# Optimization experiments

Measured on AMD Instinct MI355X. Metric: run time of the kernel, lower is better.

Reference implementation:

```python
import jax, jax.numpy as jnp
import numpy as np

B, T, D_IN, D_OUT = 2, 2048, 2048, 2048
H, KV = 32, 8
HD = D_OUT // H          # 64
G = H // KV              # group_size = 4
ROPE_BASE = 10000.0


def setup_inputs() -> dict:
    key = jax.random.key(0)
    ks = jax.random.split(key, 5)
    s = 0.02  # weight init scale
    return {
        "x":  jax.random.normal(ks[0], (B, T, D_IN), jnp.float32),
        "Wq": jax.random.normal(ks[1], (D_IN, D_OUT), jnp.float32) * s,
        "Wk": jax.random.normal(ks[2], (D_IN, KV * HD), jnp.float32) * s,
        "Wv": jax.random.normal(ks[3], (D_IN, KV * HD), jnp.float32) * s,
        "Wo": jax.random.normal(ks[4], (D_OUT, D_OUT), jnp.float32) * s,
    }


def _rope_cos_sin(t, hd):
    inv = 1.0 / (ROPE_BASE ** (jnp.arange(0, hd, 2, dtype=jnp.float32) / hd))
    ang = jnp.arange(t, dtype=jnp.float32)[:, None] * inv[None, :]  # (T, hd/2)
    return jnp.cos(ang), jnp.sin(ang)


def _apply_rope(x, cos, sin):
    # x: (b, h, T, hd); rotate adjacent pairs (complex multiply, Llama-style)
    xr = x.reshape(x.shape[:-1] + (HD // 2, 2))
    x0, x1 = xr[..., 0], xr[..., 1]
    c = cos[None, None]  # (1,1,T,hd/2)
    s = sin[None, None]
    o0 = x0 * c - x1 * s
    o1 = x0 * s + x1 * c
    return jnp.stack([o0, o1], axis=-1).reshape(x.shape)


def reference(x, Wq, Wk, Wv, Wo):
    b, t, _ = x.shape
    q = (x @ Wq).reshape(b, t, H, HD).transpose(0, 2, 1, 3)    # (b,H,T,hd)
    k = (x @ Wk).reshape(b, t, KV, HD).transpose(0, 2, 1, 3)   # (b,KV,T,hd)
    v = (x @ Wv).reshape(b, t, KV, HD).transpose(0, 2, 1, 3)
    cos, sin = _rope_cos_sin(t, HD)
    q = _apply_rope(q, cos, sin)
    k = _apply_rope(k, cos, sin)
    # GQA: expand KV groups to all heads (repeat_interleave on head dim)
    k = jnp.repeat(k, G, axis=1)  # (b,H,T,hd)
    v = jnp.repeat(v, G, axis=1)
    scores = jnp.einsum('bhqd,bhkd->bhqk', q, k) / jnp.sqrt(jnp.float32(HD))
    causal = jnp.triu(jnp.ones((t, t), dtype=bool), 1)
    scores = jnp.where(causal[None, None], -jnp.inf, scores)
    w = jax.nn.softmax(scores, axis=-1)
    ctx = jnp.einsum('bhqk,bhkd->bqhd', w, v).reshape(b, t, D_OUT)
    return ctx @ Wo
```

## Files before the change

kernel.cpp:

```cpp
#include <hip/hip_runtime.h>

#define TQ 2048
#define NB 2
#define NH 32
#define NKV 8
#define HD 64
#define DIN 2048
#define DOUT 2048
#define NQKV 3072
#define QK_W 2560
#define GK 2048

typedef unsigned short u16;
typedef unsigned int u32;
typedef __attribute__((ext_vector_type(8))) short bf16x8;
typedef __attribute__((ext_vector_type(4))) float f32x4;
typedef __attribute__((ext_vector_type(4))) u16 u16x4;

typedef __attribute__((address_space(1))) const u32 gas_u32;
typedef __attribute__((address_space(3))) u32 las_u32;

#define NEG (-1.0e30f)

__device__ __forceinline__ u16 f2bf(float f) {
  u32 u = __float_as_uint(f);
  u += 0x7fffu + ((u >> 16) & 1u);
  return (u16)(u >> 16);
}
__device__ __forceinline__ float bf2f(u16 h) { return __uint_as_float(((u32)h) << 16); }
__device__ __forceinline__ u32 pack2(float lo, float hi) {
  return (u32)f2bf(lo) | ((u32)f2bf(hi) << 16);
}

__global__ __launch_bounds__(256)
void k_cvt(const float* __restrict__ src, u16* __restrict__ dst, int n4) {
  int i = blockIdx.x * 256 + threadIdx.x;
  if (i >= n4) return;
  f32x4 v = *(const f32x4*)(src + (size_t)i * 4);
  u16x4 o;
  o[0] = f2bf(v[0]); o[1] = f2bf(v[1]); o[2] = f2bf(v[2]); o[3] = f2bf(v[3]);
  *(u16x4*)(dst + (size_t)i * 4) = o;
}

__global__ __launch_bounds__(256)
void k_transpose(const float* __restrict__ src, int nsrc, u16* __restrict__ dst, int row0) {
  __shared__ float tile[32][33];
  const int nTK = GK / 32;
  int kt = blockIdx.x % nTK, nt = blockIdx.x / nTK;
  int k0 = kt * 32, n0 = nt * 32;
  int rr = threadIdx.x >> 5, cc = threadIdx.x & 31;
#pragma unroll
  for (int p = 0; p < 4; ++p) {
    int kl = p * 8 + rr;
    tile[kl][cc] = src[(size_t)(k0 + kl) * nsrc + n0 + cc];
  }
  __syncthreads();
#pragma unroll
  for (int p = 0; p < 4; ++p) {
    int nl = p * 8 + rr;
    dst[(size_t)(row0 + n0 + nl) * GK + k0 + cc] = f2bf(tile[cc][nl]);
  }
}

__global__ __launch_bounds__(256)
void k_rope_table(float* __restrict__ tab) {
  int idx = blockIdx.x * 256 + threadIdx.x;
  int t = idx >> 5, i = idx & 31;
  float inv = 1.0f / powf(10000.0f, (float)i / 32.0f);
  float ang = (float)t * inv;
  tab[idx] = cosf(ang);
  tab[TQ * 32 + idx] = sinf(ang);
}

template <int MODE>
__global__ __launch_bounds__(256, 2)
void k_gemm(const u16* __restrict__ A, const u16* __restrict__ Bt,
            u16* __restrict__ QKV, u16* __restrict__ Vt, float* __restrict__ Cf, int N) {
  __shared__ __align__(16) u16 lds[2][16384];
  const int tid = threadIdx.x;
  const int lane = tid & 63, wid = tid >> 6;
  const int nTN = N >> 7;
  const int tm = blockIdx.x / nTN, tn = blockIdx.x % nTN;
  const int m0 = tm << 7, n0 = tn << 7;
  const int l15 = lane & 15, lg = lane >> 4;
  const int wr = (wid >> 1) << 6, wc = (wid & 1) << 6;

  f32x4 acc[4][4] = {};

  auto stage = [&](int buf, int k0) {
    u16* base = &lds[buf][0];
#pragma unroll
    for (int p = 0; p < 4; ++p) {
      int c = p * 256 + tid;
      int row = c >> 3, kb = c & 7;
      int ksrc = k0 + ((kb ^ (row & 7)) << 3);
      const u16* sA = A + (size_t)(m0 + row) * GK + ksrc;
      __builtin_amdgcn_global_load_lds((gas_u32*)sA, (las_u32*)(base + c * 8), 16, 0, 0);
      const u16* sB = Bt + (size_t)(n0 + row) * GK + ksrc;
      __builtin_amdgcn_global_load_lds((gas_u32*)sB, (las_u32*)(base + 8192 + c * 8), 16, 0, 0);
    }
  };

  auto compute = [&](int buf) {
    const u16* ldsA = &lds[buf][0];
    const u16* ldsB = &lds[buf][8192];
#pragma unroll
    for (int kk = 0; kk < 2; ++kk) {
      bf16x8 af[4], bfr[4];
#pragma unroll
      for (int m = 0; m < 4; ++m) {
        int row = wr + m * 16 + l15;
        int koff = (kk * 32 + lg * 8) ^ ((row & 7) << 3);
        af[m] = *(const bf16x8*)(ldsA + row * 64 + koff);
      }
#pragma unroll
      for (int n = 0; n < 4; ++n) {
        int row = wc + n * 16 + l15;
        int koff = (kk * 32 + lg * 8) ^ ((row & 7) << 3);
        bfr[n] = *(const bf16x8*)(ldsB + row * 64 + koff);
      }
#pragma unroll
      for (int m = 0; m < 4; ++m)
#pragma unroll
        for (int n = 0; n < 4; ++n)
          acc[m][n] = __builtin_amdgcn_mfma_f32_16x16x32_bf16(af[m], bfr[n], acc[m][n], 0, 0, 0);
    }
  };

  stage(0, 0);
  __syncthreads();
  const int nk = GK / 64;
  for (int t = 0; t < nk; ++t) {
    if (t + 1 < nk) stage((t + 1) & 1, (t + 1) * 64);
    compute(t & 1);
    __syncthreads();
  }

  if (MODE == 1) {
#pragma unroll
    for (int m = 0; m < 4; ++m)
#pragma unroll
      for (int n = 0; n < 4; ++n)
#pragma unroll
        for (int r = 0; r < 4; ++r) {
          int row = m0 + wr + m * 16 + lg * 4 + r;
          int col = n0 + wc + n * 16 + l15;
          Cf[(size_t)row * N + col] = acc[m][n][r];
        }
  } else if (n0 >= 2560) {
#pragma unroll
    for (int m = 0; m < 4; ++m)
#pragma unroll
      for (int n = 0; n < 4; ++n)
#pragma unroll
        for (int r = 0; r < 4; ++r) {
          int row = m0 + wr + m * 16 + lg * 4 + r;
          int col = n0 + wc + n * 16 + l15;
          int dh = col - 2560, kvh = dh >> 6, d = dh & 63;
          int bb = row >> 11, tt = row & 2047;
          Vt[(((size_t)bb * NKV + kvh) * 64 + d) * TQ + tt] = f2bf(acc[m][n][r]);
        }
  } else {
#pragma unroll
    for (int m = 0; m < 4; ++m)
#pragma unroll
      for (int n = 0; n < 4; ++n)
#pragma unroll
        for (int r = 0; r < 4; ++r) {
          int row = m0 + wr + m * 16 + lg * 4 + r;
          int col = n0 + wc + n * 16 + l15;
          QKV[(size_t)row * QK_W + col] = f2bf(acc[m][n][r]);
        }
  }
}

__global__ __launch_bounds__(256)
void k_rope(u16* __restrict__ QKV, const float* __restrict__ tab) {
  int idx = blockIdx.x * 256 + threadIdx.x;
  const int perRow = QK_W / 8;
  int row = idx / perRow, c0 = (idx % perRow) * 8;
  int t = row & (TQ - 1);
  int d0 = c0 & 63;
  u16* p = QKV + (size_t)row * QK_W + c0;
  bf16x8 v = *(const bf16x8*)p;
  const float* ct = tab + t * 32 + (d0 >> 1);
  const float* st = tab + TQ * 32 + t * 32 + (d0 >> 1);
  bf16x8 o;
#pragma unroll
  for (int j = 0; j < 4; ++j) {
    float x0 = bf2f((u16)v[2 * j]), x1 = bf2f((u16)v[2 * j + 1]);
    float cc = ct[j], ss = st[j];
    o[2 * j]     = (short)f2bf(x0 * cc - x1 * ss);
    o[2 * j + 1] = (short)f2bf(x0 * ss + x1 * cc);
  }
  *(bf16x8*)p = o;
}

__global__ __launch_bounds__(256, 3)
void k_attn(const u16* __restrict__ QKV, const u16* __restrict__ Vt, u16* __restrict__ ctx) {
  __shared__ __align__(16) u16 Ksh[2][4096];
  __shared__ __align__(16) u16 Vsh[2][4096];
  __shared__ __align__(16) u16 Psh[4][2048];
  const int tid = threadIdx.x, lane = tid & 63, w = tid >> 6;
  const int l15 = lane & 15, lg = lane >> 4;
  const int bid = blockIdx.x;
  const int qt = 15 - (bid >> 6);
  const int hb = bid & 63;
  const int h = hb & 31, b = hb >> 5;
  const int kvh = h >> 2;
  const int q0 = qt << 7;
  const int qb = q0 + w * 32;
  const size_t rowbase = (size_t)b * TQ;
  const u16* Vg = Vt + ((size_t)(b * NKV + kvh)) * 64 * TQ;

  auto stage = [&](int buf, int kv0) {
    u16* kd = &Ksh[buf][0];
    u16* vd = &Vsh[buf][0];
#pragma unroll
    for (int p = 0; p < 2; ++p) {
      int c = p * 256 + tid;
      int row = c >> 3, kb = c & 7;
      int off = (kb ^ (row & 7)) << 3;
      const u16* sK = QKV + (rowbase + kv0 + row) * QK_W + 2048 + kvh * 64 + off;
      __builtin_amdgcn_global_load_lds((gas_u32*)sK, (las_u32*)(kd + c * 8), 16, 0, 0);
      const u16* sV = Vg + (size_t)row * TQ + kv0 + off;
      __builtin_amdgcn_global_load_lds((gas_u32*)sV, (las_u32*)(vd + c * 8), 16, 0, 0);
    }
  };

  bf16x8 qf[2][2];
#pragma unroll
  for (int m = 0; m < 2; ++m)
#pragma unroll
    for (int kk = 0; kk < 2; ++kk)
      qf[m][kk] = *(const bf16x8*)(QKV + (rowbase + qb + m * 16 + l15) * QK_W + h * 64 + kk * 32 + lg * 8);

  float m_run[2] = {NEG, NEG}, l_run[2] = {0.f, 0.f};
  f32x4 oacc[2][4] = {};

  stage(0, 0);
  const int nt = 2 * qt + 2;
  for (int t = 0; t < nt; ++t) {
    const int kv0 = t << 6;
    __syncthreads();
    if (t + 1 < nt) stage((t + 1) & 1, kv0 + 64);
    if (kv0 > qb + 31) continue;

    const u16* Kl = &Ksh[t & 1][0];
    const u16* Vl = &Vsh[t & 1][0];

    f32x4 stv[2][4];
#pragma unroll
    for (int c = 0; c < 4; ++c) {
      const int krow = c * 16 + l15;
      const int ks = (krow & 7) << 3;
      f32x4 z0 = {}, z1 = {};
#pragma unroll
      for (int kk = 0; kk < 2; ++kk) {
        bf16x8 kf = *(const bf16x8*)(Kl + krow * 64 + ((kk * 32 + lg * 8) ^ ks));
        z0 = __builtin_amdgcn_mfma_f32_16x16x32_bf16(kf, qf[0][kk], z0, 0, 0, 0);
        z1 = __builtin_amdgcn_mfma_f32_16x16x32_bf16(kf, qf[1][kk], z1, 0, 0, 0);
      }
      stv[0][c] = z0; stv[1][c] = z1;
    }

    const bool maskT = (kv0 + 63 > qb);
    float mt[2];
#pragma unroll
    for (int m = 0; m < 2; ++m) {
      const int qpos = qb + m * 16 + l15;
      float mx = NEG;
#pragma unroll
      for (int c = 0; c < 4; ++c)
#pragma unroll
        for (int r = 0; r < 4; ++r) {
          float sv = stv[m][c][r] * 0.125f;
          if (maskT) {
            int kvpos = kv0 + c * 16 + lg * 4 + r;
            sv = (kvpos > qpos) ? NEG : sv;
          }
          stv[m][c][r] = sv;
          mx = fmaxf(mx, sv);
        }
      mx = fmaxf(mx, __shfl_xor(mx, 16));
      mx = fmaxf(mx, __shfl_xor(mx, 32));
      mt[m] = mx;
    }

#pragma unroll
    for (int m = 0; m < 2; ++m) {
      float nm = fmaxf(m_run[m], mt[m]);
      float sc = __expf(m_run[m] - nm);
      m_run[m] = nm;
      l_run[m] *= sc;
#pragma unroll
      for (int dt = 0; dt < 4; ++dt) oacc[m][dt] *= sc;
    }

    u16* Pw = &Psh[w][0];
#pragma unroll
    for (int m = 0; m < 2; ++m) {
      float ssum = 0.f;
      const int rowp = m * 16 + l15;
      const int swz = (l15 & 7) << 3;
#pragma unroll
      for (int c = 0; c < 4; ++c) {
        float p0 = __expf(stv[m][c][0] - m_run[m]);
        float p1 = __expf(stv[m][c][1] - m_run[m]);
        float p2 = __expf(stv[m][c][2] - m_run[m]);
        float p3 = __expf(stv[m][c][3] - m_run[m]);
        ssum += (p0 + p1) + (p2 + p3);
        const int kvb = (c * 16 + lg * 4) ^ swz;
        *(u32*)(Pw + rowp * 64 + kvb)       = pack2(p0, p1);
        *(u32*)(Pw + rowp * 64 + (kvb | 2)) = pack2(p2, p3);
      }
      ssum += __shfl_xor(ssum, 16);
      ssum += __shfl_xor(ssum, 32);
      l_run[m] += ssum;
    }

    bf16x8 pf[2][2];
#pragma unroll
    for (int m = 0; m < 2; ++m)
#pragma unroll
      for (int kc = 0; kc < 2; ++kc)
        pf[m][kc] = *(const bf16x8*)(Pw + (m * 16 + l15) * 64 + ((kc * 32 + lg * 8) ^ ((l15 & 7) << 3)));
#pragma unroll
    for (int dt = 0; dt < 4; ++dt) {
      const int vrow = dt * 16 + l15;
      const int vs = (vrow & 7) << 3;
#pragma unroll
      for (int kc = 0; kc < 2; ++kc) {
        bf16x8 vf = *(const bf16x8*)(Vl + vrow * 64 + ((kc * 32 + lg * 8) ^ vs));
        oacc[0][dt] = __builtin_amdgcn_mfma_f32_16x16x32_bf16(vf, pf[0][kc], oacc[0][dt], 0, 0, 0);
        oacc[1][dt] = __builtin_amdgcn_mfma_f32_16x16x32_bf16(vf, pf[1][kc], oacc[1][dt], 0, 0, 0);
      }
    }
  }

#pragma unroll
  for (int m = 0; m < 2; ++m) {
    float inv = 1.0f / l_run[m];
    size_t row = rowbase + qb + m * 16 + l15;
#pragma unroll
    for (int dt = 0; dt < 4; ++dt) {
      int col = h * 64 + dt * 16 + lg * 4;
      u32 w0 = pack2(oacc[m][dt][0] * inv, oacc[m][dt][1] * inv);
      u32 w1 = pack2(oacc[m][dt][2] * inv, oacc[m][dt][3] * inv);
      *(u32*)(ctx + row * DOUT + col) = w0;
      *(u32*)(ctx + row * DOUT + col + 2) = w1;
    }
  }
}

extern "C" void kernel_launch(void* const* d_in, const int* in_sizes, int n_in,
                              void* d_out, int out_size, void* d_ws, size_t ws_size,
                              hipStream_t stream) {
  const float* x  = (const float*)d_in[0];
  const float* Wq = (const float*)d_in[1];
  const float* Wk = (const float*)d_in[2];
  const float* Wv = (const float*)d_in[3];
  const float* Wo = (const float*)d_in[4];
  float* out = (float*)d_out;

  char* ws = (char*)d_ws;
  size_t off = 0;
  auto alloc = [&](size_t bytes) -> void* {
    void* p = ws + off;
    off += (bytes + 255) & ~(size_t)255;
    return p;
  };
  const int rows = NB * TQ;
  u16*   xb    = (u16*)alloc((size_t)rows * DIN * 2);
  u16*   WqkvT = (u16*)alloc((size_t)NQKV * GK * 2);
  u16*   WoT   = (u16*)alloc((size_t)DOUT * GK * 2);
  u16*   QKV   = (u16*)alloc((size_t)rows * QK_W * 2);
  u16*   Vt    = (u16*)alloc((size_t)NB * NKV * 64 * TQ * 2);
  u16*   ctx   = (u16*)alloc((size_t)rows * DOUT * 2);
  float* tab   = (float*)alloc((size_t)2 * TQ * 32 * 4);

  k_cvt<<<dim3(rows * DIN / 4 / 256), dim3(256), 0, stream>>>(x, xb, rows * DIN / 4);
  k_transpose<<<dim3((GK / 32) * (2048 / 32)), dim3(256), 0, stream>>>(Wq, 2048, WqkvT, 0);
  k_transpose<<<dim3((GK / 32) * (512 / 32)),  dim3(256), 0, stream>>>(Wk, 512,  WqkvT, 2048);
  k_transpose<<<dim3((GK / 32) * (512 / 32)),  dim3(256), 0, stream>>>(Wv, 512,  WqkvT, 2560);
  k_transpose<<<dim3((GK / 32) * (2048 / 32)), dim3(256), 0, stream>>>(Wo, 2048, WoT, 0);
  k_rope_table<<<dim3(TQ * 32 / 256), dim3(256), 0, stream>>>(tab);

  k_gemm<0><<<dim3((rows / 128) * (NQKV / 128)), dim3(256), 0, stream>>>(xb, WqkvT, QKV, Vt, nullptr, NQKV);
  k_rope<<<dim3(rows * (QK_W / 8) / 256), dim3(256), 0, stream>>>(QKV, tab);
  k_attn<<<dim3(NB * NH * (TQ / 128)), dim3(256), 0, stream>>>(QKV, Vt, ctx);
  k_gemm<1><<<dim3((rows / 128) * (DOUT / 128)), dim3(256), 0, stream>>>(ctx, WoT, nullptr, nullptr, out, DOUT);
}
```

Baseline: 210.3 us.

## Fuse RoPE into QKV GEMM epilogue and streamline attention softmax

Applies RoPE inside the QKV GEMM epilogue, using a lane shuffle to fetch the paired element and an interleaved cos/sin table, and removes the separate rope kernel along with its QKV read-write pass. In attention, the softmax switches to base-2 exponentials via v_exp_f32 with the 1/sqrt(d) scale folded into the constant, splits the masked and unmasked max paths, and rescales the running max only when some row's max exceeds it by a threshold. Packing to bf16 now uses the hardware v_cvt_pk_bf16_f32 instruction. The lazy rescale lets exponents grow before rescaling, and the epilogue rope rounds the fp32 accumulator once rather than twice.

```diff
diff --git a/kernel.cpp b/kernel.cpp
--- a/kernel.cpp
+++ b/kernel.cpp
@@ -21,6 +21,7 @@
 typedef __attribute__((address_space(3))) u32 las_u32;
 
 #define NEG (-1.0e30f)
+#define CL2 0.18033688f
 
 __device__ __forceinline__ u16 f2bf(float f) {
   u32 u = __float_as_uint(f);
@@ -28,8 +29,15 @@
   return (u16)(u >> 16);
 }
 __device__ __forceinline__ float bf2f(u16 h) { return __uint_as_float(((u32)h) << 16); }
-__device__ __forceinline__ u32 pack2(float lo, float hi) {
-  return (u32)f2bf(lo) | ((u32)f2bf(hi) << 16);
+__device__ __forceinline__ u32 cvtpk(float lo, float hi) {
+  u32 r;
+  asm("v_cvt_pk_bf16_f32 %0, %1, %2" : "=v"(r) : "v"(lo), "v"(hi));
+  return r;
+}
+__device__ __forceinline__ float exp2g(float x) {
+  float r;
+  asm("v_exp_f32 %0, %1\n\ts_nop 0" : "=v"(r) : "v"(x));
+  return r;
 }
 
 __global__ __launch_bounds__(256)
@@ -63,19 +71,19 @@
 }
 
 __global__ __launch_bounds__(256)
-void k_rope_table(float* __restrict__ tab) {
+void k_rope_table(float2* __restrict__ tab) {
   int idx = blockIdx.x * 256 + threadIdx.x;
   int t = idx >> 5, i = idx & 31;
   float inv = 1.0f / powf(10000.0f, (float)i / 32.0f);
   float ang = (float)t * inv;
-  tab[idx] = cosf(ang);
-  tab[TQ * 32 + idx] = sinf(ang);
+  tab[idx] = make_float2(cosf(ang), sinf(ang));
 }
 
 template <int MODE>
 __global__ __launch_bounds__(256, 2)
 void k_gemm(const u16* __restrict__ A, const u16* __restrict__ Bt,
-            u16* __restrict__ QKV, u16* __restrict__ Vt, float* __restrict__ Cf, int N) {
+            u16* __restrict__ QKV, u16* __restrict__ Vt, float* __restrict__ Cf,
+            const float2* __restrict__ tab, int N) {
   __shared__ __align__(16) u16 lds[2][16384];
   const int tid = threadIdx.x;
   const int lane = tid & 63, wid = tid >> 6;
@@ -164,36 +172,22 @@
 #pragma unroll
     for (int m = 0; m < 4; ++m)
 #pragma unroll
-      for (int n = 0; n < 4; ++n)
+      for (int n = 0; n < 4; ++n) {
+        int col = n0 + wc + n * 16 + l15;
+        int dh = (col & 63) >> 1;
+        float sgn = (col & 1) ? 1.0f : -1.0f;
 #pragma unroll
         for (int r = 0; r < 4; ++r) {
           int row = m0 + wr + m * 16 + lg * 4 + r;
-          int col = n0 + wc + n * 16 + l15;
-          QKV[(size_t)row * QK_W + col] = f2bf(acc[m][n][r]);
+          float a = acc[m][n][r];
+          float b = __shfl_xor(a, 1);
+          int t = row & (TQ - 1);
+          float2 csv = tab[t * 32 + dh];
+          float o = a * csv.x + sgn * b * csv.y;
+          QKV[(size_t)row * QK_W + col] = f2bf(o);
         }
-  }
-}
-
-__global__ __launch_bounds__(256)
-void k_rope(u16* __restrict__ QKV, const float* __restrict__ tab) {
-  int idx = blockIdx.x * 256 + threadIdx.x;
-  const int perRow = QK_W / 8;
-  int row = idx / perRow, c0 = (idx % perRow) * 8;
-  int t = row & (TQ - 1);
-  int d0 = c0 & 63;
-  u16* p = QKV + (size_t)row * QK_W + c0;
-  bf16x8 v = *(const bf16x8*)p;
-  const float* ct = tab + t * 32 + (d0 >> 1);
-  const float* st = tab + TQ * 32 + t * 32 + (d0 >> 1);
-  bf16x8 o;
-#pragma unroll
-  for (int j = 0; j < 4; ++j) {
-    float x0 = bf2f((u16)v[2 * j]), x1 = bf2f((u16)v[2 * j + 1]);
-    float cc = ct[j], ss = st[j];
-    o[2 * j]     = (short)f2bf(x0 * cc - x1 * ss);
-    o[2 * j + 1] = (short)f2bf(x0 * ss + x1 * cc);
-  }
-  *(bf16x8*)p = o;
+      }
+  }
 }
 
 __global__ __launch_bounds__(256, 3)
@@ -266,53 +260,69 @@
 
     const bool maskT = (kv0 + 63 > qb);
     float mt[2];
+    if (maskT) {
+#pragma unroll
+      for (int m = 0; m < 2; ++m) {
+        const int qpos = qb + m * 16 + l15;
+        float mx = NEG;
+#pragma unroll
+        for (int c = 0; c < 4; ++c)
+#pragma unroll
+          for (int r = 0; r < 4; ++r) {
+            int kvpos = kv0 + c * 16 + lg * 4 + r;
+            float sv = stv[m][c][r];
+            sv = (kvpos > qpos) ? NEG : sv;
+            stv[m][c][r] = sv;
+            mx = fmaxf(mx, sv);
+          }
+        mt[m] = mx;
+      }
+    } else {
+#pragma unroll
+      for (int m = 0; m < 2; ++m) {
+        float mx = NEG;
+#pragma unroll
+        for (int c = 0; c < 4; ++c)
+#pragma unroll
+          for (int r = 0; r < 4; ++r) mx = fmaxf(mx, stv[m][c][r]);
+        mt[m] = mx;
+      }
+    }
 #pragma unroll
     for (int m = 0; m < 2; ++m) {
-      const int qpos = qb + m * 16 + l15;
-      float mx = NEG;
-#pragma unroll
-      for (int c = 0; c < 4; ++c)
-#pragma unroll
-        for (int r = 0; r < 4; ++r) {
-          float sv = stv[m][c][r] * 0.125f;
-          if (maskT) {
-            int kvpos = kv0 + c * 16 + lg * 4 + r;
-            sv = (kvpos > qpos) ? NEG : sv;
-          }
-          stv[m][c][r] = sv;
-          mx = fmaxf(mx, sv);
-        }
-      mx = fmaxf(mx, __shfl_xor(mx, 16));
-      mx = fmaxf(mx, __shfl_xor(mx, 32));
-      mt[m] = mx;
-    }
-
+      mt[m] = fmaxf(mt[m], __shfl_xor(mt[m], 16));
+      mt[m] = fmaxf(mt[m], __shfl_xor(mt[m], 32));
+    }
+
+    if (__any((mt[0] > m_run[0] + 64.0f) || (mt[1] > m_run[1] + 64.0f))) {
+#pragma unroll
+      for (int m = 0; m < 2; ++m) {
+        float nm = fmaxf(m_run[m], mt[m]);
+        float sc = exp2g((m_run[m] - nm) * CL2);
+        m_run[m] = nm;
+        l_run[m] *= sc;
+#pragma unroll
+        for (int dt = 0; dt < 4; ++dt) oacc[m][dt] *= sc;
+      }
+    }
+
+    u16* Pw = &Psh[w][0];
 #pragma unroll
     for (int m = 0; m < 2; ++m) {
-      float nm = fmaxf(m_run[m], mt[m]);
-      float sc = __expf(m_run[m] - nm);
-      m_run[m] = nm;
-      l_run[m] *= sc;
-#pragma unroll
-      for (int dt = 0; dt < 4; ++dt) oacc[m][dt] *= sc;
-    }
-
-    u16* Pw = &Psh[w][0];
-#pragma unroll
-    for (int m = 0; m < 2; ++m) {
+      const float msc = m_run[m] * CL2;
       float ssum = 0.f;
       const int rowp = m * 16 + l15;
       const int swz = (l15 & 7) << 3;
 #pragma unroll
       for (int c = 0; c < 4; ++c) {
-        float p0 = __expf(stv[m][c][0] - m_run[m]);
-        float p1 = __expf(stv[m][c][1] - m_run[m]);
-        float p2 = __expf(stv[m][c][2] - m_run[m]);
-        float p3 = __expf(stv[m][c][3] - m_run[m]);
+        float p0 = exp2g(stv[m][c][0] * CL2 - msc);
+        float p1 = exp2g(stv[m][c][1] * CL2 - msc);
+        float p2 = exp2g(stv[m][c][2] * CL2 - msc);
+        float p3 = exp2g(stv[m][c][3] * CL2 - msc);
         ssum += (p0 + p1) + (p2 + p3);
         const int kvb = (c * 16 + lg * 4) ^ swz;
-        *(u32*)(Pw + rowp * 64 + kvb)       = pack2(p0, p1);
-        *(u32*)(Pw + rowp * 64 + (kvb | 2)) = pack2(p2, p3);
+        *(u32*)(Pw + rowp * 64 + kvb)       = cvtpk(p0, p1);
+        *(u32*)(Pw + rowp * 64 + (kvb | 2)) = cvtpk(p2, p3);
       }
       ssum += __shfl_xor(ssum, 16);
       ssum += __shfl_xor(ssum, 32);
@@ -345,8 +355,8 @@
 #pragma unroll
     for (int dt = 0; dt < 4; ++dt) {
       int col = h * 64 + dt * 16 + lg * 4;
-      u32 w0 = pack2(oacc[m][dt][0] * inv, oacc[m][dt][1] * inv);
-      u32 w1 = pack2(oacc[m][dt][2] * inv, oacc[m][dt][3] * inv);
+      u32 w0 = cvtpk(oacc[m][dt][0] * inv, oacc[m][dt][1] * inv);
+      u32 w1 = cvtpk(oacc[m][dt][2] * inv, oacc[m][dt][3] * inv);
       *(u32*)(ctx + row * DOUT + col) = w0;
       *(u32*)(ctx + row * DOUT + col + 2) = w1;
     }
@@ -371,13 +381,13 @@
     return p;
   };
   const int rows = NB * TQ;
-  u16*   xb    = (u16*)alloc((size_t)rows * DIN * 2);
-  u16*   WqkvT = (u16*)alloc((size_t)NQKV * GK * 2);
-  u16*   WoT   = (u16*)alloc((size_t)DOUT * GK * 2);
-  u16*   QKV   = (u16*)alloc((size_t)rows * QK_W * 2);
-  u16*   Vt    = (u16*)alloc((size_t)NB * NKV * 64 * TQ * 2);
-  u16*   ctx   = (u16*)alloc((size_t)rows * DOUT * 2);
-  float* tab   = (float*)alloc((size_t)2 * TQ * 32 * 4);
+  u16*    xb    = (u16*)alloc((size_t)rows * DIN * 2);
+  u16*    WqkvT = (u16*)alloc((size_t)NQKV * GK * 2);
+  u16*    WoT   = (u16*)alloc((size_t)DOUT * GK * 2);
+  u16*    QKV   = (u16*)alloc((size_t)rows * QK_W * 2);
+  u16*    Vt    = (u16*)alloc((size_t)NB * NKV * 64 * TQ * 2);
+  u16*    ctx   = (u16*)alloc((size_t)rows * DOUT * 2);
+  float2* tab   = (float2*)alloc((size_t)TQ * 32 * sizeof(float2));
 
   k_cvt<<<dim3(rows * DIN / 4 / 256), dim3(256), 0, stream>>>(x, xb, rows * DIN / 4);
   k_transpose<<<dim3((GK / 32) * (2048 / 32)), dim3(256), 0, stream>>>(Wq, 2048, WqkvT, 0);
@@ -386,8 +396,7 @@
   k_transpose<<<dim3((GK / 32) * (2048 / 32)), dim3(256), 0, stream>>>(Wo, 2048, WoT, 0);
   k_rope_table<<<dim3(TQ * 32 / 256), dim3(256), 0, stream>>>(tab);
 
-  k_gemm<0><<<dim3((rows / 128) * (NQKV / 128)), dim3(256), 0, stream>>>(xb, WqkvT, QKV, Vt, nullptr, NQKV);
-  k_rope<<<dim3(rows * (QK_W / 8) / 256), dim3(256), 0, stream>>>(QKV, tab);
+  k_gemm<0><<<dim3((rows / 128) * (NQKV / 128)), dim3(256), 0, stream>>>(xb, WqkvT, QKV, Vt, nullptr, tab, NQKV);
   k_attn<<<dim3(NB * NH * (TQ / 128)), dim3(256), 0, stream>>>(QKV, Vt, ctx);
-  k_gemm<1><<<dim3((rows / 128) * (DOUT / 128)), dim3(256), 0, stream>>>(ctx, WoT, nullptr, nullptr, out, DOUT);
-}
+  k_gemm<1><<<dim3((rows / 128) * (DOUT / 128)), dim3(256), 0, stream>>>(ctx, WoT, nullptr, nullptr, out, nullptr, DOUT);
+}
```

After: 191.9 us. 8.8% less time.
